# Performance work log

Hardware: AMD Instinct MI355X
Metric: run time of the kernel (lower is better)

The kernel has to match this reference:

```python
import jax, jax.numpy as jnp
import numpy as np

B, NPG, H, HEADS, L, E, IN_DIM, FREQ = 4, 256, 128, 4, 6, 65536, 5, 256
N = B * NPG
C = H // HEADS  # per-head channels = 32


def _w(key, shape, fan_in):
    return jax.random.normal(key, shape, jnp.float32) * (fan_in ** -0.5)


def _ln(x):  # LayerNorm, elementwise_affine=False, eps=1e-5
    mu = jnp.mean(x, axis=-1, keepdims=True)
    var = jnp.mean((x - mu) ** 2, axis=-1, keepdims=True)
    return (x - mu) / jnp.sqrt(var + 1e-5)


def setup_inputs() -> dict:
    key = jax.random.key(0)
    ks = jax.random.split(key, 40)
    x = jax.random.normal(ks[0], (N, IN_DIM), jnp.float32)
    # edges constrained within each graph
    kg = jnp.repeat(jnp.arange(B), E // B)
    src = jax.random.randint(ks[1], (E,), 0, NPG) + kg * NPG
    dst = jax.random.randint(ks[2], (E,), 0, NPG) + kg * NPG
    edge_index = jnp.stack([src, dst]).astype(jnp.int32)
    batch = jnp.repeat(jnp.arange(B), NPG).astype(jnp.int32)
    time_matrix = jax.random.normal(ks[3], (N, N), jnp.float32)
    p = {}
    p['Wn'] = _w(ks[4], (IN_DIM, H), IN_DIM); p['bn'] = jnp.zeros((H,), jnp.float32)
    p['Wee'] = _w(ks[5], (1, 1), 1); p['bee'] = jnp.zeros((1,), jnp.float32)
    p['Wt1'] = _w(ks[6], (FREQ, H), FREQ); p['bt1'] = jnp.zeros((H,), jnp.float32)
    p['Wt2'] = _w(ks[7], (H, H), H); p['bt2'] = jnp.zeros((H,), jnp.float32)
    p['Wa'] = _w(ks[8], (L, H, 4 * H), H); p['ba'] = jnp.zeros((L, 4 * H), jnp.float32)
    p['Wq'] = _w(ks[9], (L, H, H), H); p['bq'] = jnp.zeros((L, H), jnp.float32)
    p['Wk'] = _w(ks[10], (L, H, H), H); p['bk'] = jnp.zeros((L, H), jnp.float32)
    p['Wv'] = _w(ks[11], (L, H, H), H); p['bv'] = jnp.zeros((L, H), jnp.float32)
    p['We'] = _w(ks[12], (L, 1, H), 1)  # lin_edge, bias=False in PyG
    p['Wskip'] = _w(ks[13], (L, H, H), H); p['bskip'] = jnp.zeros((L, H), jnp.float32)
    p['Wf1'] = _w(ks[14], (L, H, 2 * H), H); p['bf1'] = jnp.zeros((L, 2 * H), jnp.float32)
    p['Wf2'] = _w(ks[15], (L, 2 * H, H), 2 * H); p['bf2'] = jnp.zeros((L, H), jnp.float32)
    p['Wb'] = _w(ks[16], (H, H, H), H); p['bb'] = jnp.zeros((H,), jnp.float32)
    p['Wm1'] = _w(ks[17], (H, H), H); p['bm1'] = jnp.zeros((H,), jnp.float32)
    p['Wm2'] = _w(ks[18], (H, 4), H); p['bm2'] = jnp.zeros((4,), jnp.float32)
    return {'x': x, 'edge_index': edge_index, 'batch': batch, 't': 50,
            'time_matrix': time_matrix, **p}


def reference(x, edge_index, batch, t, time_matrix,
              Wn, bn, Wee, bee, Wt1, bt1, Wt2, bt2,
              Wa, ba, Wq, bq, Wk, bk, Wv, bv, We, Wskip, bskip,
              Wf1, bf1, Wf2, bf2, Wb, bb, Wm1, bm1, Wm2, bm2):
    h = x @ Wn + bn  # [N,H]
    # sinusoidal timestep embedding (dim=FREQ)
    half = FREQ // 2
    freqs = jnp.exp(-jnp.log(jnp.float32(10000.0)) * jnp.arange(half, dtype=jnp.float32) / half)
    targs = jnp.float32(t) * freqs
    emb = jnp.concatenate([jnp.cos(targs), jnp.sin(targs)])[None, :]  # [1,FREQ]
    t_emb = jax.nn.silu(emb @ Wt1 + bt1) @ Wt2 + bt2  # [1,H]
    t_mod = jax.nn.silu(t_emb)

    src, dst = edge_index[0], edge_index[1]
    edge_attr = time_matrix[src, dst][:, None] @ Wee + bee  # [E,1]

    inv_sqrt_c = jnp.float32(1.0 / np.sqrt(C))
    for l in range(L):
        ss = t_mod @ Wa[l] + ba[l]  # [1,4H]
        sh_msa, sc_msa, sh_mlp, sc_mlp = jnp.split(ss, 4, axis=1)
        hn = _ln(h) * (1 + sc_msa) + sh_msa
        # TransformerConv: gather per-edge Q/K/V, softmax over incoming edges of dst
        q = (hn @ Wq[l] + bq[l]).reshape(N, HEADS, C)
        k = (hn @ Wk[l] + bk[l]).reshape(N, HEADS, C)
        v = (hn @ Wv[l] + bv[l]).reshape(N, HEADS, C)
        e = (edge_attr @ We[l]).reshape(E, HEADS, C)
        kj = k[src] + e
        alpha = jnp.sum(q[dst] * kj, axis=-1) * inv_sqrt_c  # [E,HEADS]
        m = jax.ops.segment_max(alpha, dst, num_segments=N)
        a = jnp.exp(alpha - m[dst])
        s = jax.ops.segment_sum(a, dst, num_segments=N)
        a = a / (s[dst] + 1e-16)
        msg = (v[src] + e) * a[..., None]  # [E,HEADS,C]
        attn_out = jax.ops.segment_sum(msg, dst, num_segments=N).reshape(N, H)
        attn_out = attn_out + hn @ Wskip[l] + bskip[l]  # root/skip connection
        h = h + attn_out
        hn = _ln(h) * (1 + sc_mlp) + sh_mlp
        h = h + (jax.nn.gelu(hn @ Wf1[l] + bf1[l], approximate=False) @ Wf2[l] + bf2[l])

    # to_dense_batch: all graphs have NPG nodes -> reshape, full mask
    hd = h.reshape(B, NPG, H)
    # nn.Bilinear: pair[b,i,j,o] = h[b,i] @ Wb[o] @ h[b,j] + bb[o]
    tmp = jnp.einsum('bik,okl->biol', hd, Wb)  # [B,n,H,H]
    pair = jnp.einsum('biol,bjl->bijo', tmp, hd) + bb  # [B,n,n,H]
    logits = jax.nn.silu(pair @ Wm1 + bm1) @ Wm2 + bm2  # [B,n,n,4]
    return logits
```

## Files before the change

kernel.cpp:

```cpp
#include <hip/hip_runtime.h>
#include <math.h>

#define N_NODES 1024
#define HDIM 128
#define EDGES 65536
#define LAYERS 6

typedef __attribute__((ext_vector_type(8))) short bf16x8;
typedef __attribute__((ext_vector_type(4))) float f32x4;

#define OFF_H     0
#define OFF_Q     131072
#define OFF_K     262144
#define OFF_V     393216
#define OFF_SKP   524288
#define OFF_G     655360
#define OFF_SS    917504
#define OFF_EA    920576
#define OFF_CVEC  986112
#define OFF_INT   986240
#define OFF_M     1054912
#define OFF_U     3152064
#define OFF_MT    11540672
#define OFF_HB    12589248
#define OFF_TMOD  12654784
#define OFF_WB    12654912

__device__ __forceinline__ float silu_f(float x) { return x / (1.f + expf(-x)); }
__device__ __forceinline__ float frcp(float x) { return __builtin_amdgcn_rcpf(x); }

__device__ __forceinline__ unsigned short f2bf(float f) {
    unsigned int u = __float_as_uint(f);
    u += 0x7FFFu + ((u >> 16) & 1u);
    return (unsigned short)(u >> 16);
}

__global__ __launch_bounds__(1024) void k_tmod(const void* tptr,
    const float* __restrict__ Wt1, const float* __restrict__ bt1,
    const float* __restrict__ Wt2, const float* __restrict__ bt2,
    const float* __restrict__ bb, const float* __restrict__ Wm1, const float* __restrict__ bm1,
    float* __restrict__ tmod_g, float* __restrict__ cvec)
{
    __shared__ float emb_s[256];
    __shared__ float part[8][128];
    __shared__ float tmp1_s[128];
    int tid = threadIdx.x;
    int iv = *(const int*)tptr;
    float fv = __int_as_float(iv);
    float tval = (iv > -1000000 && iv < 1000000) ? (float)iv : fv;
    if (tid < 256) {
        int fi = tid & 127;
        float fr = expf(-logf(10000.f) * (float)fi / 128.f);
        float ta = tval * fr;
        emb_s[tid] = (tid < 128) ? cosf(ta) : sinf(ta);
    }
    __syncthreads();
    {
        int col = tid & 127, sl = tid >> 7;
        float p = 0.f;
#pragma unroll 8
        for (int i = sl * 32; i < sl * 32 + 32; i++) p += emb_s[i] * Wt1[i * 128 + col];
        part[sl][col] = p;
    }
    __syncthreads();
    if (tid < 128) {
        float a = bt1[tid];
#pragma unroll
        for (int s = 0; s < 8; s++) a += part[s][tid];
        tmp1_s[tid] = silu_f(a);
    }
    __syncthreads();
    {
        int col = tid & 127, sl = tid >> 7;
        float p = 0.f;
#pragma unroll 8
        for (int i = sl * 16; i < sl * 16 + 16; i++) p += tmp1_s[i] * Wt2[i * 128 + col];
        part[sl][col] = p;
    }
    __syncthreads();
    if (tid < 128) {
        float a = bt2[tid];
#pragma unroll
        for (int s = 0; s < 8; s++) a += part[s][tid];
        tmod_g[tid] = silu_f(a);
    }
    __syncthreads();
    {
        int col = tid & 127, sl = tid >> 7;
        float p = 0.f;
#pragma unroll 8
        for (int i = sl * 16; i < sl * 16 + 16; i++) p += bb[i] * Wm1[i * 128 + col];
        part[sl][col] = p;
    }
    __syncthreads();
    if (tid < 128) {
        float a = bm1[tid];
#pragma unroll
        for (int s = 0; s < 8; s++) a += part[s][tid];
        cvec[tid] = a;
    }
}

__global__ __launch_bounds__(256) void k_ss(const float* __restrict__ tmod_g,
    const float* __restrict__ Wa, const float* __restrict__ ba, float* __restrict__ ss_all)
{
    __shared__ float tm_s[128];
    int tid = threadIdx.x;
    if (tid < 128) tm_s[tid] = tmod_g[tid];
    __syncthreads();
    int idx = blockIdx.x * 256 + tid;
    int l = idx >> 9, j = idx & 511;
    float a = ba[l * 512 + j];
    const float* w = Wa + l * 65536 + j;
#pragma unroll 4
    for (int k = 0; k < 128; k++) a += tm_s[k] * w[k * 512];
    ss_all[idx] = a;
}

__global__ __launch_bounds__(256) void k_wtrans(
    const float* __restrict__ Wq, const float* __restrict__ Wk,
    const float* __restrict__ Wv, const float* __restrict__ Wsk,
    const float* __restrict__ Wf1, const float* __restrict__ Wf2,
    short* __restrict__ WT)
{
    __shared__ __align__(16) short T[64][80];
    int t = blockIdx.x;
    int tid = threadIdx.x;
    const float* src; short* dst; int K, N, kt, nt;
    if (t < 96) {
        int mat = t >> 2, sub = t & 3;
        int l = mat >> 2, m = mat & 3;
        src = (m == 0 ? Wq : m == 1 ? Wk : m == 2 ? Wv : Wsk) + l * 16384;
        dst = WT + (size_t)mat * 16384;
        K = 128; N = 128; kt = sub >> 1; nt = sub & 1;
    } else if (t < 144) {
        int i = t - 96; int l = i >> 3, sub = i & 7;
        src = Wf1 + l * 32768;
        dst = WT + 24 * 16384 + (size_t)l * 32768;
        K = 128; N = 256; kt = sub & 1; nt = sub >> 1;
    } else {
        int i = t - 144; int l = i >> 3, sub = i & 7;
        src = Wf2 + l * 32768;
        dst = WT + 24 * 16384 + 6 * 32768 + (size_t)l * 32768;
        K = 256; N = 128; kt = sub >> 1; nt = sub & 1;
    }
    int k0 = kt * 64, n0 = nt * 64;
    for (int p = 0; p < 16; p++) {
        int idx = p * 256 + tid;
        int kk = idx >> 6, nn = idx & 63;
        T[nn][kk] = (short)f2bf(src[(k0 + kk) * N + n0 + nn]);
    }
    __syncthreads();
    for (int p = 0; p < 2; p++) {
        int idx = p * 256 + tid;
        int nn = idx >> 3, sq = idx & 7;
        *(int4*)&dst[(size_t)(n0 + nn) * K + k0 + sq * 8] = *(const int4*)&T[nn][sq * 8];
    }
}

__global__ __launch_bounds__(256) void k_input(const float* __restrict__ x,
    const float* __restrict__ Wn, const float* __restrict__ bn, float* __restrict__ h)
{
    int idx = blockIdx.x * 256 + threadIdx.x;
    int i = idx >> 7, j = idx & 127;
    float acc = bn[j];
#pragma unroll
    for (int kk = 0; kk < 5; kk++) acc += x[i * 5 + kk] * Wn[kk * 128 + j];
    h[idx] = acc;
}

__global__ __launch_bounds__(256) void k_edge_count(const int* __restrict__ ei,
    const float* __restrict__ tm, const float* __restrict__ Wee, const float* __restrict__ bee,
    float* __restrict__ ea, int* __restrict__ deg)
{
    int e = blockIdx.x * 256 + threadIdx.x;
    int s = ei[e], d = ei[EDGES + e];
    ea[e] = tm[s * N_NODES + d] * Wee[0] + bee[0];
    atomicAdd(&deg[d], 1);
}

__global__ __launch_bounds__(1024) void k_scan(const int* __restrict__ deg, int* __restrict__ rowptr)
{
    __shared__ int tmp[1024];
    int tid = threadIdx.x;
    tmp[tid] = deg[tid];
    __syncthreads();
    for (int off = 1; off < 1024; off <<= 1) {
        int vv = (tid >= off) ? tmp[tid - off] : 0;
        __syncthreads();
        tmp[tid] += vv;
        __syncthreads();
    }
    rowptr[tid + 1] = tmp[tid];
    if (tid == 0) rowptr[0] = 0;
}

__global__ __launch_bounds__(256) void k_scatter(const int* __restrict__ ei,
    const int* __restrict__ rowptr, int* __restrict__ cursor, int* __restrict__ eorder)
{
    int e = blockIdx.x * 256 + threadIdx.x;
    int d = ei[EDGES + e];
    int pos = atomicAdd(&cursor[d], 1);
    eorder[rowptr[d] + pos] = e;
}

__global__ __launch_bounds__(128) void k_sort2(const int* __restrict__ rowptr,
    int* __restrict__ eorder, const int* __restrict__ ei, const float* __restrict__ ea,
    int* __restrict__ src_csr, float* __restrict__ ea_csr)
{
    __shared__ int key[256];
    int node = blockIdx.x;
    int tid = threadIdx.x;
    int beg = rowptr[node], end = rowptr[node + 1];
    int n = end - beg;
    if (n <= 256) {
        for (int i = tid; i < 256; i += 128) key[i] = (i < n) ? eorder[beg + i] : 0x7FFFFFFF;
        __syncthreads();
        for (int k = 2; k <= 256; k <<= 1) {
            for (int j = k >> 1; j > 0; j >>= 1) {
                int i = ((tid / j) * 2 * j) + (tid % j);
                int l = i + j;
                bool up = ((i & k) == 0);
                int a = key[i], b = key[l];
                if ((a > b) == up) { key[i] = b; key[l] = a; }
                __syncthreads();
            }
        }
        for (int i = tid; i < n; i += 128) {
            int e = key[i];
            src_csr[beg + i] = ei[e];
            ea_csr[beg + i] = ea[e];
        }
    } else {
        if (tid == 0) {
            for (int i = beg + 1; i < end; ++i) {
                int kk = eorder[i];
                int j = i - 1;
                while (j >= beg && eorder[j] > kk) { eorder[j + 1] = eorder[j]; --j; }
                eorder[j + 1] = kk;
            }
        }
        __syncthreads();
        for (int i = tid; i < n; i += 128) {
            int e = eorder[beg + i];
            src_csr[beg + i] = ei[e];
            ea_csr[beg + i] = ea[e];
        }
    }
}

__global__ __launch_bounds__(256) void k_qkvs(const float* __restrict__ h,
    const float* __restrict__ ss, const short* __restrict__ WT, int layer,
    const float* __restrict__ bq, const float* __restrict__ bk,
    const float* __restrict__ bv, const float* __restrict__ bsk,
    float* __restrict__ q, float* __restrict__ k, float* __restrict__ v, float* __restrict__ skp)
{
    __shared__ __align__(16) short As[32][136];
    __shared__ float shs[128], scs[128];
    int tid = threadIdx.x;
    int r0 = blockIdx.x * 32;
    int mat = blockIdx.y;
    if (tid < 128) { shs[tid] = ss[tid]; scs[tid] = ss[128 + tid]; }
    __syncthreads();
    {
        int row = tid >> 3, o = tid & 7;
        const float* hr = h + (size_t)(r0 + row) * 128 + o * 16;
        float s = 0.f, s2 = 0.f;
#pragma unroll
        for (int j = 0; j < 4; j++) {
            float4 vv = *(const float4*)&hr[j * 4];
            s += vv.x + vv.y + vv.z + vv.w;
            s2 += vv.x * vv.x + vv.y * vv.y + vv.z * vv.z + vv.w * vv.w;
        }
        s += __shfl_xor(s, 1, 64); s2 += __shfl_xor(s2, 1, 64);
        s += __shfl_xor(s, 2, 64); s2 += __shfl_xor(s2, 2, 64);
        s += __shfl_xor(s, 4, 64); s2 += __shfl_xor(s2, 4, 64);
        float mu = s * (1.f / 128.f);
        float var = s2 * (1.f / 128.f) - mu * mu;
        float rs = rsqrtf(var + 1e-5f);
#pragma unroll
        for (int j = 0; j < 4; j++) {
            float4 vv = *(const float4*)&hr[j * 4];
            int cb = o * 16 + j * 4;
            short4 o4;
            o4.x = (short)f2bf((vv.x - mu) * rs * (1.f + scs[cb])     + shs[cb]);
            o4.y = (short)f2bf((vv.y - mu) * rs * (1.f + scs[cb + 1]) + shs[cb + 1]);
            o4.z = (short)f2bf((vv.z - mu) * rs * (1.f + scs[cb + 2]) + shs[cb + 2]);
            o4.w = (short)f2bf((vv.w - mu) * rs * (1.f + scs[cb + 3]) + shs[cb + 3]);
            *(short4*)&As[row][cb] = o4;
        }
    }
    __syncthreads();
    int w = tid >> 6, lane = tid & 63, c = lane & 15, g = lane >> 4;
    const short* Wm = WT + (size_t)(layer * 4 + mat) * 16384;
    f32x4 acc[2][2] = {};
#pragma unroll
    for (int kq = 0; kq < 4; kq++) {
        int ko = kq * 32 + g * 8;
        bf16x8 a0 = *(const bf16x8*)&As[c][ko];
        bf16x8 a1 = *(const bf16x8*)&As[16 + c][ko];
#pragma unroll
        for (int nt = 0; nt < 2; nt++) {
            bf16x8 bfr = *(const bf16x8*)&Wm[(size_t)(w * 32 + nt * 16 + c) * 128 + ko];
            acc[0][nt] = __builtin_amdgcn_mfma_f32_16x16x32_bf16(a0, bfr, acc[0][nt], 0, 0, 0);
            acc[1][nt] = __builtin_amdgcn_mfma_f32_16x16x32_bf16(a1, bfr, acc[1][nt], 0, 0, 0);
        }
    }
    const float* bias; float* out;
    switch (mat) {
        case 0:  bias = bq;  out = q;   break;
        case 1:  bias = bk;  out = k;   break;
        case 2:  bias = bv;  out = v;   break;
        default: bias = bsk; out = skp; break;
    }
#pragma unroll
    for (int it = 0; it < 2; it++)
#pragma unroll
        for (int nt = 0; nt < 2; nt++) {
            int n = w * 32 + nt * 16 + c;
            float bv2 = bias[n];
#pragma unroll
            for (int r = 0; r < 4; r++) {
                int i = r0 + it * 16 + g * 4 + r;
                out[(size_t)i * 128 + n] = acc[it][nt][r] + bv2;
            }
        }
}

__global__ __launch_bounds__(256) void k_ffn(float* __restrict__ h,
    const short* __restrict__ WT, int layer,
    const float* __restrict__ bf1, const float* __restrict__ bf2,
    const float* __restrict__ ss2, short* __restrict__ hb, int last)
{
    __shared__ __align__(16) short As[16][136];
    __shared__ __align__(16) short Gs[16][264];
    __shared__ float shs[128], scs[128];
    int tid = threadIdx.x;
    int r0 = blockIdx.x * 16;
    if (tid < 128) { shs[tid] = ss2[tid]; scs[tid] = ss2[128 + tid]; }
    __syncthreads();
    {
        int row = tid >> 4, o = tid & 15;
        const float* hr = h + (size_t)(r0 + row) * 128 + o * 8;
        float s = 0.f, s2 = 0.f;
#pragma unroll
        for (int j = 0; j < 2; j++) {
            float4 vv = *(const float4*)&hr[j * 4];
            s += vv.x + vv.y + vv.z + vv.w;
            s2 += vv.x * vv.x + vv.y * vv.y + vv.z * vv.z + vv.w * vv.w;
        }
        s += __shfl_xor(s, 1, 64); s2 += __shfl_xor(s2, 1, 64);
        s += __shfl_xor(s, 2, 64); s2 += __shfl_xor(s2, 2, 64);
        s += __shfl_xor(s, 4, 64); s2 += __shfl_xor(s2, 4, 64);
        s += __shfl_xor(s, 8, 64); s2 += __shfl_xor(s2, 8, 64);
        float mu = s * (1.f / 128.f);
        float var = s2 * (1.f / 128.f) - mu * mu;
        float rs = rsqrtf(var + 1e-5f);
#pragma unroll
        for (int j = 0; j < 2; j++) {
            float4 vv = *(const float4*)&hr[j * 4];
            int cb = o * 8 + j * 4;
            short4 o4;
            o4.x = (short)f2bf((vv.x - mu) * rs * (1.f + scs[cb])     + shs[cb]);
            o4.y = (short)f2bf((vv.y - mu) * rs * (1.f + scs[cb + 1]) + shs[cb + 1]);
            o4.z = (short)f2bf((vv.z - mu) * rs * (1.f + scs[cb + 2]) + shs[cb + 2]);
            o4.w = (short)f2bf((vv.w - mu) * rs * (1.f + scs[cb + 3]) + shs[cb + 3]);
            *(short4*)&As[row][cb] = o4;
        }
    }
    __syncthreads();
    int w = tid >> 6, lane = tid & 63, c = lane & 15, g = lane >> 4;
    const short* W1 = WT + 24 * 16384 + (size_t)layer * 32768;
    const short* W2 = WT + 24 * 16384 + 6 * 32768 + (size_t)layer * 32768;
    {
        f32x4 acc[4] = {};
#pragma unroll
        for (int kq = 0; kq < 4; kq++) {
            int ko = kq * 32 + g * 8;
            bf16x8 a0 = *(const bf16x8*)&As[c][ko];
#pragma unroll
            for (int nt = 0; nt < 4; nt++) {
                bf16x8 bfr = *(const bf16x8*)&W1[(size_t)(w * 64 + nt * 16 + c) * 128 + ko];
                acc[nt] = __builtin_amdgcn_mfma_f32_16x16x32_bf16(a0, bfr, acc[nt], 0, 0, 0);
            }
        }
#pragma unroll
        for (int nt = 0; nt < 4; nt++) {
            int n = w * 64 + nt * 16 + c;
            float bv = bf1[n];
#pragma unroll
            for (int r = 0; r < 4; r++) {
                float y = acc[nt][r] + bv;
                float gl = 0.5f * y * (1.f + erff(y * 0.70710678118654752f));
                Gs[g * 4 + r][n] = (short)f2bf(gl);
            }
        }
    }
    __syncthreads();
    {
        f32x4 acc2[2] = {};
#pragma unroll
        for (int kq = 0; kq < 8; kq++) {
            int ko = kq * 32 + g * 8;
            bf16x8 a0 = *(const bf16x8*)&Gs[c][ko];
#pragma unroll
            for (int nt2 = 0; nt2 < 2; nt2++) {
                bf16x8 bfr = *(const bf16x8*)&W2[(size_t)(w * 32 + nt2 * 16 + c) * 256 + ko];
                acc2[nt2] = __builtin_amdgcn_mfma_f32_16x16x32_bf16(a0, bfr, acc2[nt2], 0, 0, 0);
            }
        }
#pragma unroll
        for (int nt2 = 0; nt2 < 2; nt2++) {
            int n = w * 32 + nt2 * 16 + c;
            float bv = bf2[n];
#pragma unroll
            for (int r = 0; r < 4; r++) {
                int i = r0 + g * 4 + r;
                float nv = h[(size_t)i * 128 + n] + acc2[nt2][r] + bv;
                h[(size_t)i * 128 + n] = nv;
                if (last) hb[(size_t)i * 128 + n] = (short)f2bf(nv);
            }
        }
    }
}

__global__ __launch_bounds__(256) void k_attn(const float* __restrict__ q,
    const float* __restrict__ k, const float* __restrict__ v,
    const float* __restrict__ skp, float* __restrict__ h,
    const int* __restrict__ src_csr, const float* __restrict__ ea_csr,
    const float* __restrict__ We_l, const int* __restrict__ rowptr)
{
    __shared__ float ms[2][64], ssb[2][64], a0s[2][64], a1s[2][64];
    int tid = threadIdx.x;
    int wid = tid >> 6;
    int lane = tid & 63;
    int nslot = wid >> 1;
    int half = wid & 1;
    int node = blockIdx.x * 2 + nslot;
    int c0 = lane * 2;
    float2 q2 = *(const float2*)&q[node * 128 + c0];
    float we0 = We_l[c0], we1 = We_l[c0 + 1];
    int beg = rowptr[node], end = rowptr[node + 1];
    int n = end - beg;
    int mid = beg + ((n + 1) >> 1);
    int tb = half ? mid : beg;
    int te = half ? end : mid;
    float m = -INFINITY, s = 0.f, a0 = 0.f, a1 = 0.f;
    const float isc = 0.17677669529663687f;

    int t = tb;
    for (; t + 3 < te; t += 4) {
        int sn0 = src_csr[t],     sn1 = src_csr[t + 1];
        int sn2 = src_csr[t + 2], sn3 = src_csr[t + 3];
        float e0 = ea_csr[t],     e1 = ea_csr[t + 1];
        float e2 = ea_csr[t + 2], e3 = ea_csr[t + 3];
        float2 k0 = *(const float2*)&k[sn0 * 128 + c0];
        float2 k1 = *(const float2*)&k[sn1 * 128 + c0];
        float2 k2 = *(const float2*)&k[sn2 * 128 + c0];
        float2 k3 = *(const float2*)&k[sn3 * 128 + c0];
        float2 v0 = *(const float2*)&v[sn0 * 128 + c0];
        float2 v1 = *(const float2*)&v[sn1 * 128 + c0];
        float2 v2 = *(const float2*)&v[sn2 * 128 + c0];
        float2 v3 = *(const float2*)&v[sn3 * 128 + c0];
        float p0 = q2.x * (k0.x + e0 * we0) + q2.y * (k0.y + e0 * we1);
        float p1 = q2.x * (k1.x + e1 * we0) + q2.y * (k1.y + e1 * we1);
        float p2 = q2.x * (k2.x + e2 * we0) + q2.y * (k2.y + e2 * we1);
        float p3 = q2.x * (k3.x + e3 * we0) + q2.y * (k3.y + e3 * we1);
        p0 += __shfl_xor(p0, 1, 16); p1 += __shfl_xor(p1, 1, 16);
        p2 += __shfl_xor(p2, 1, 16); p3 += __shfl_xor(p3, 1, 16);
        p0 += __shfl_xor(p0, 2, 16); p1 += __shfl_xor(p1, 2, 16);
        p2 += __shfl_xor(p2, 2, 16); p3 += __shfl_xor(p3, 2, 16);
        p0 += __shfl_xor(p0, 4, 16); p1 += __shfl_xor(p1, 4, 16);
        p2 += __shfl_xor(p2, 4, 16); p3 += __shfl_xor(p3, 4, 16);
        p0 += __shfl_xor(p0, 8, 16); p1 += __shfl_xor(p1, 8, 16);
        p2 += __shfl_xor(p2, 8, 16); p3 += __shfl_xor(p3, 8, 16);
        {
            float al = p0 * isc;
            float mn = fmaxf(m, al);
            float scale = __expf(m - mn), wq = __expf(al - mn);
            s = s * scale + wq;
            a0 = a0 * scale + wq * (v0.x + e0 * we0);
            a1 = a1 * scale + wq * (v0.y + e0 * we1);
            m = mn;
        }
        {
            float al = p1 * isc;
            float mn = fmaxf(m, al);
            float scale = __expf(m - mn), wq = __expf(al - mn);
            s = s * scale + wq;
            a0 = a0 * scale + wq * (v1.x + e1 * we0);
            a1 = a1 * scale + wq * (v1.y + e1 * we1);
            m = mn;
        }
        {
            float al = p2 * isc;
            float mn = fmaxf(m, al);
            float scale = __expf(m - mn), wq = __expf(al - mn);
            s = s * scale + wq;
            a0 = a0 * scale + wq * (v2.x + e2 * we0);
            a1 = a1 * scale + wq * (v2.y + e2 * we1);
            m = mn;
        }
        {
            float al = p3 * isc;
            float mn = fmaxf(m, al);
            float scale = __expf(m - mn), wq = __expf(al - mn);
            s = s * scale + wq;
            a0 = a0 * scale + wq * (v3.x + e3 * we0);
            a1 = a1 * scale + wq * (v3.y + e3 * we1);
            m = mn;
        }
    }
    for (; t < te; ++t) {
        int sn = src_csr[t];
        float eav = ea_csr[t];
        float2 kv = *(const float2*)&k[sn * 128 + c0];
        float2 vv = *(const float2*)&v[sn * 128 + c0];
        float part = q2.x * (kv.x + eav * we0) + q2.y * (kv.y + eav * we1);
        part += __shfl_xor(part, 1, 16);
        part += __shfl_xor(part, 2, 16);
        part += __shfl_xor(part, 4, 16);
        part += __shfl_xor(part, 8, 16);
        float alpha = part * isc;
        float mn = fmaxf(m, alpha);
        float scale = __expf(m - mn), wq = __expf(alpha - mn);
        s = s * scale + wq;
        a0 = a0 * scale + wq * (vv.x + eav * we0);
        a1 = a1 * scale + wq * (vv.y + eav * we1);
        m = mn;
    }
    if (half == 1) {
        ms[nslot][lane] = m; ssb[nslot][lane] = s;
        a0s[nslot][lane] = a0; a1s[nslot][lane] = a1;
    }
    __syncthreads();
    if (half == 0) {
        float mB = ms[nslot][lane], sB = ssb[nslot][lane];
        float b0 = a0s[nslot][lane], b1 = a1s[nslot][lane];
        float mm = fmaxf(m, mB);
        float eA = (m  > -1e30f) ? __expf(m  - mm) : 0.f;
        float eB = (mB > -1e30f) ? __expf(mB - mm) : 0.f;
        float sT = s * eA + sB * eB;
        float o0 = a0 * eA + b0 * eB;
        float o1 = a1 * eA + b1 * eB;
        float inv = (sT > 0.f) ? 1.f / (sT + 1e-16f) : 0.f;
        int o = node * 128 + c0;
        h[o]     += skp[o]     + o0 * inv;
        h[o + 1] += skp[o + 1] + o1 * inv;
    }
}

__global__ __launch_bounds__(256) void k_mprep(const float* __restrict__ Wb,
    const float* __restrict__ Wm1, float* __restrict__ M)
{
    __shared__ float wb_s[64][128];
    __shared__ float wm_s[64][128];
    int tid = threadIdx.x;
    int k = blockIdx.x;
    int mg = tid & 15, lg = tid >> 4;
    int m0 = mg * 8, l0 = lg * 8;
    float acc[8][8] = {};
    for (int oh = 0; oh < 2; ++oh) {
        __syncthreads();
        for (int idx = tid; idx < 8192; idx += 256) {
            int o = idx >> 7, c = idx & 127;
            wb_s[o][c] = Wb[(size_t)(oh * 64 + o) * 16384 + k * 128 + c];
            wm_s[o][c] = Wm1[(oh * 64 + o) * 128 + c];
        }
        __syncthreads();
        for (int o = 0; o < 64; o++) {
            float lv[8], mv[8];
#pragma unroll
            for (int i = 0; i < 8; i++) { lv[i] = wb_s[o][l0 + i]; mv[i] = wm_s[o][m0 + i]; }
#pragma unroll
            for (int li = 0; li < 8; li++)
#pragma unroll
                for (int mi = 0; mi < 8; mi++) acc[li][mi] += lv[li] * mv[mi];
        }
    }
    for (int mi = 0; mi < 8; mi++)
        for (int li = 0; li < 8; li++)
            M[(size_t)k * 16384 + (m0 + mi) * 128 + (l0 + li)] = acc[li][mi];
}

__global__ __launch_bounds__(256) void k_mtrans(const float* __restrict__ M,
                                                short* __restrict__ Mt)
{
    __shared__ __align__(16) short Ts[64][136];
    int tid = threadIdx.x;
    int n0 = blockIdx.x * 64;
    for (int p = 0; p < 32; p++) {
        int idx = p * 256 + tid;
        int k = idx >> 6, nn = idx & 63;
        Ts[nn][k] = (short)f2bf(M[(size_t)k * 16384 + n0 + nn]);
    }
    __syncthreads();
    for (int p = 0; p < 4; p++) {
        int idx = p * 256 + tid;
        int nn = idx >> 4, s = idx & 15;
        *(int4*)&Mt[(size_t)(n0 + nn) * 128 + s * 8] = *(const int4*)&Ts[nn][s * 8];
    }
}

__global__ __launch_bounds__(256) void k_p1(const short* __restrict__ hb,
    const short* __restrict__ Mt, short* __restrict__ U)
{
    __shared__ __align__(16) short As[128][72];
    __shared__ __align__(16) short Bs[128][72];
    int tid = threadIdx.x;
    int n0 = blockIdx.x * 128;
    int i0 = blockIdx.y * 128;
    int w = tid >> 6, lane = tid & 63, c = lane & 15, g = lane >> 4;
    f32x4 acc[2][8] = {};
    for (int kh = 0; kh < 2; kh++) {
        __syncthreads();
        for (int idx = tid; idx < 1024; idx += 256) {
            int r = idx >> 3, s = idx & 7;
            *(int4*)&As[r][s * 8] = *(const int4*)&hb[(i0 + r) * 128 + kh * 64 + s * 8];
            *(int4*)&Bs[r][s * 8] = *(const int4*)&Mt[(size_t)(n0 + r) * 128 + kh * 64 + s * 8];
        }
        __syncthreads();
#pragma unroll
        for (int kk = 0; kk < 2; kk++) {
            int ko = kk * 32 + g * 8;
            bf16x8 a0 = *(const bf16x8*)&As[w * 32 + c][ko];
            bf16x8 a1 = *(const bf16x8*)&As[w * 32 + 16 + c][ko];
#pragma unroll
            for (int nt = 0; nt < 8; nt++) {
                bf16x8 b = *(const bf16x8*)&Bs[nt * 16 + c][ko];
                acc[0][nt] = __builtin_amdgcn_mfma_f32_16x16x32_bf16(a0, b, acc[0][nt], 0, 0, 0);
                acc[1][nt] = __builtin_amdgcn_mfma_f32_16x16x32_bf16(a1, b, acc[1][nt], 0, 0, 0);
            }
        }
    }
#pragma unroll
    for (int it = 0; it < 2; it++)
#pragma unroll
        for (int nt = 0; nt < 8; nt++)
#pragma unroll
            for (int r = 0; r < 4; r++) {
                int i = i0 + w * 32 + it * 16 + g * 4 + r;
                int n = n0 + nt * 16 + c;
                U[(size_t)i * 16384 + n] = (short)f2bf(acc[it][nt][r]);
            }
}

__global__ __launch_bounds__(256) void k_p2(const short* __restrict__ hb,
    const short* __restrict__ U, const float* __restrict__ cvec,
    const float* __restrict__ Wm2, const float* __restrict__ bm2,
    float* __restrict__ out)
{
    __shared__ __align__(16) short Us[128][136];
    __shared__ float cvs[128];
    __shared__ float w2s[128][4];
    int tid = threadIdx.x;
    int i = blockIdx.x;
    int jb = blockIdx.y;
    int b = i >> 8;
    int w = tid >> 6, lane = tid & 63, c = lane & 15, g = lane >> 4;
    if (tid < 128) {
        cvs[tid] = cvec[tid];
        *(float4*)&w2s[tid][0] = *(const float4*)&Wm2[tid * 4];
    }
    bf16x8 hf[2][4];
    {
        const short* hrow = hb + (size_t)(b * 256 + jb * 128 + w * 32 + c) * 128;
#pragma unroll
        for (int jt = 0; jt < 2; jt++)
#pragma unroll
            for (int kq = 0; kq < 4; kq++)
                hf[jt][kq] = *(const bf16x8*)(hrow + jt * 16 * 128 + kq * 32 + g * 8);
    }
    for (int idx = tid; idx < 2048; idx += 256) {
        int r = idx >> 4, s = idx & 15;
        *(int4*)&Us[r][s * 8] = *(const int4*)&U[(size_t)i * 16384 + r * 128 + s * 8];
    }
    __syncthreads();
    f32x4 acc[2][8] = {};
#pragma unroll
    for (int kq = 0; kq < 4; kq++) {
        int ko = kq * 32 + g * 8;
#pragma unroll
        for (int mt = 0; mt < 8; mt++) {
            bf16x8 uv = *(const bf16x8*)&Us[mt * 16 + c][ko];
            acc[0][mt] = __builtin_amdgcn_mfma_f32_16x16x32_bf16(uv, hf[0][kq], acc[0][mt], 0, 0, 0);
            acc[1][mt] = __builtin_amdgcn_mfma_f32_16x16x32_bf16(uv, hf[1][kq], acc[1][mt], 0, 0, 0);
        }
    }
    float4 bmv = *(const float4*)&bm2[0];
#pragma unroll
    for (int jt = 0; jt < 2; jt++) {
        float p0 = 0.f, p1 = 0.f, p2 = 0.f, p3 = 0.f;
#pragma unroll
        for (int mt = 0; mt < 8; mt++) {
#pragma unroll
            for (int r = 0; r < 4; r++) {
                int m = mt * 16 + g * 4 + r;
                float y = acc[jt][mt][r] + cvs[m];
                float sv = y * frcp(1.f + __expf(-y));
                p0 += sv * w2s[m][0]; p1 += sv * w2s[m][1];
                p2 += sv * w2s[m][2]; p3 += sv * w2s[m][3];
            }
        }
        p0 += __shfl_xor(p0, 16, 64); p1 += __shfl_xor(p1, 16, 64);
        p2 += __shfl_xor(p2, 16, 64); p3 += __shfl_xor(p3, 16, 64);
        p0 += __shfl_xor(p0, 32, 64); p1 += __shfl_xor(p1, 32, 64);
        p2 += __shfl_xor(p2, 32, 64); p3 += __shfl_xor(p3, 32, 64);
        if (g == 0) {
            int j = jb * 128 + w * 32 + jt * 16 + c;
            float4 o4 = { p0 + bmv.x, p1 + bmv.y, p2 + bmv.z, p3 + bmv.w };
            *(float4*)&out[((size_t)i * 256 + j) * 4] = o4;
        }
    }
}

extern "C" void kernel_launch(void* const* d_in, const int* in_sizes, int n_in,
                              void* d_out, int out_size, void* d_ws, size_t ws_size,
                              hipStream_t stream)
{
    const float* x   = (const float*)d_in[0];
    const int*   ei  = (const int*)d_in[1];
    const void*  tptr= d_in[3];
    const float* tm  = (const float*)d_in[4];
    const float* Wn  = (const float*)d_in[5];
    const float* bn  = (const float*)d_in[6];
    const float* Wee = (const float*)d_in[7];
    const float* bee = (const float*)d_in[8];
    const float* Wt1 = (const float*)d_in[9];
    const float* bt1 = (const float*)d_in[10];
    const float* Wt2 = (const float*)d_in[11];
    const float* bt2 = (const float*)d_in[12];
    const float* Wa  = (const float*)d_in[13];
    const float* ba  = (const float*)d_in[14];
    const float* Wq  = (const float*)d_in[15];
    const float* bq  = (const float*)d_in[16];
    const float* Wk  = (const float*)d_in[17];
    const float* bk  = (const float*)d_in[18];
    const float* Wv  = (const float*)d_in[19];
    const float* bv  = (const float*)d_in[20];
    const float* We  = (const float*)d_in[21];
    const float* Wsk = (const float*)d_in[22];
    const float* bsk = (const float*)d_in[23];
    const float* Wf1 = (const float*)d_in[24];
    const float* bf1 = (const float*)d_in[25];
    const float* Wf2 = (const float*)d_in[26];
    const float* bf2 = (const float*)d_in[27];
    const float* Wb  = (const float*)d_in[28];
    const float* bb  = (const float*)d_in[29];
    const float* Wm1 = (const float*)d_in[30];
    const float* bm1 = (const float*)d_in[31];
    const float* Wm2 = (const float*)d_in[32];
    const float* bm2 = (const float*)d_in[33];
    float* out = (float*)d_out;
    float* ws = (float*)d_ws;

    float* h    = ws + OFF_H;
    float* qb   = ws + OFF_Q;
    float* kb   = ws + OFF_K;
    float* vb   = ws + OFF_V;
    float* skp  = ws + OFF_SKP;
    float* ss   = ws + OFF_SS;
    float* ea   = ws + OFF_EA;
    float* cvec = ws + OFF_CVEC;
    int* iws    = (int*)(ws + OFF_INT);
    int* deg    = iws;
    int* cursor = iws + 1024;
    int* rowptr = iws + 2048;
    int* eorder = iws + 3073;
    int* src_csr   = (int*)(ws + OFF_G);
    float* ea_csr  = ws + OFF_G + 65536;
    float* Mst  = ws + OFF_M;
    short* Ub   = (short*)(ws + OFF_U);
    short* Mtb  = (short*)(ws + OFF_MT);
    short* hbb  = (short*)(ws + OFF_HB);
    float* tmod = ws + OFF_TMOD;
    short* WT   = (short*)(ws + OFF_WB);

    hipMemsetAsync(deg, 0, 2048 * sizeof(int), stream);
    k_tmod<<<1, 1024, 0, stream>>>(tptr, Wt1, bt1, Wt2, bt2, bb, Wm1, bm1, tmod, cvec);
    k_ss<<<12, 256, 0, stream>>>(tmod, Wa, ba, ss);
    k_wtrans<<<192, 256, 0, stream>>>(Wq, Wk, Wv, Wsk, Wf1, Wf2, WT);
    k_input<<<512, 256, 0, stream>>>(x, Wn, bn, h);
    k_edge_count<<<256, 256, 0, stream>>>(ei, tm, Wee, bee, ea, deg);
    k_scan<<<1, 1024, 0, stream>>>(deg, rowptr);
    k_scatter<<<256, 256, 0, stream>>>(ei, rowptr, cursor, eorder);
    k_sort2<<<1024, 128, 0, stream>>>(rowptr, eorder, ei, ea, src_csr, ea_csr);

    for (int l = 0; l < LAYERS; l++) {
        const float* ssl = ss + l * 512;
        k_qkvs<<<dim3(32, 4), 256, 0, stream>>>(h, ssl, WT, l,
            bq + l * 128, bk + l * 128, bv + l * 128, bsk + l * 128,
            qb, kb, vb, skp);
        k_attn<<<512, 256, 0, stream>>>(qb, kb, vb, skp, h, src_csr, ea_csr,
                                        We + l * 128, rowptr);
        k_ffn<<<64, 256, 0, stream>>>(h, WT, l, bf1 + l * 256, bf2 + l * 128,
                                      ssl + 256, hbb, l == LAYERS - 1);
    }

    k_mprep<<<128, 256, 0, stream>>>(Wb, Wm1, Mst);
    k_mtrans<<<256, 256, 0, stream>>>(Mst, Mtb);
    k_p1<<<dim3(128, 8), 256, 0, stream>>>(hbb, Mtb, Ub);
    k_p2<<<dim3(1024, 2), 256, 0, stream>>>(hbb, Ub, cvec, Wm2, bm2, out);
}
```

Measured before the change: 286.8 us.

## Fuse setup kernels, split attention per node over four waves, use MFMA for bilinear prep

Merges the time-embedding and scale/shift kernels into one 12-block launch, and the input projection and edge-count kernels into one launch, to cut launch overhead. Each node's attention now gets a whole block, with its edges split across four waves and merged by online softmax. The bilinear weight precompute becomes a bf16 MFMA GEMM that reads a transposed bf16 Wm1 written by the weight-transpose kernel. Each fused setup block recomputes the time MLP redundantly, and bf16 lowers the precision of the bilinear weights.

```diff
diff --git a/kernel.cpp b/kernel.cpp
--- a/kernel.cpp
+++ b/kernel.cpp
@@ -26,6 +26,8 @@
 #define OFF_TMOD  12654784
 #define OFF_WB    12654912
 
+#define WM1T_OFF  786432
+
 __device__ __forceinline__ float silu_f(float x) { return x / (1.f + expf(-x)); }
 __device__ __forceinline__ float frcp(float x) { return __builtin_amdgcn_rcpf(x); }
 
@@ -35,20 +37,22 @@
     return (unsigned short)(u >> 16);
 }
 
-__global__ __launch_bounds__(1024) void k_tmod(const void* tptr,
+__global__ __launch_bounds__(256) void k_ssf(const void* tptr,
     const float* __restrict__ Wt1, const float* __restrict__ bt1,
     const float* __restrict__ Wt2, const float* __restrict__ bt2,
     const float* __restrict__ bb, const float* __restrict__ Wm1, const float* __restrict__ bm1,
-    float* __restrict__ tmod_g, float* __restrict__ cvec)
+    const float* __restrict__ Wa, const float* __restrict__ ba,
+    float* __restrict__ ss_all, float* __restrict__ cvec)
 {
     __shared__ float emb_s[256];
-    __shared__ float part[8][128];
+    __shared__ float part[2][128];
     __shared__ float tmp1_s[128];
+    __shared__ float tmod_s[128];
     int tid = threadIdx.x;
     int iv = *(const int*)tptr;
     float fv = __int_as_float(iv);
     float tval = (iv > -1000000 && iv < 1000000) ? (float)iv : fv;
-    if (tid < 256) {
+    {
         int fi = tid & 127;
         float fr = expf(-logf(10000.f) * (float)fi / 128.f);
         float ta = tval * fr;
@@ -59,69 +63,49 @@
         int col = tid & 127, sl = tid >> 7;
         float p = 0.f;
 #pragma unroll 8
-        for (int i = sl * 32; i < sl * 32 + 32; i++) p += emb_s[i] * Wt1[i * 128 + col];
+        for (int i = sl * 128; i < sl * 128 + 128; i++) p += emb_s[i] * Wt1[i * 128 + col];
         part[sl][col] = p;
     }
     __syncthreads();
-    if (tid < 128) {
-        float a = bt1[tid];
-#pragma unroll
-        for (int s = 0; s < 8; s++) a += part[s][tid];
-        tmp1_s[tid] = silu_f(a);
-    }
+    if (tid < 128) tmp1_s[tid] = silu_f(bt1[tid] + part[0][tid] + part[1][tid]);
     __syncthreads();
     {
         int col = tid & 127, sl = tid >> 7;
         float p = 0.f;
 #pragma unroll 8
-        for (int i = sl * 16; i < sl * 16 + 16; i++) p += tmp1_s[i] * Wt2[i * 128 + col];
+        for (int i = sl * 64; i < sl * 64 + 64; i++) p += tmp1_s[i] * Wt2[i * 128 + col];
         part[sl][col] = p;
     }
     __syncthreads();
-    if (tid < 128) {
-        float a = bt2[tid];
-#pragma unroll
-        for (int s = 0; s < 8; s++) a += part[s][tid];
-        tmod_g[tid] = silu_f(a);
-    }
-    __syncthreads();
-    {
-        int col = tid & 127, sl = tid >> 7;
-        float p = 0.f;
+    if (tid < 128) tmod_s[tid] = silu_f(bt2[tid] + part[0][tid] + part[1][tid]);
+    __syncthreads();
+    {
+        int idx = blockIdx.x * 256 + tid;
+        int l = idx >> 9, j = idx & 511;
+        float a = ba[l * 512 + j];
+        const float* w = Wa + l * 65536 + j;
+#pragma unroll 4
+        for (int k = 0; k < 128; k++) a += tmod_s[k] * w[k * 512];
+        ss_all[idx] = a;
+    }
+    if (blockIdx.x == 0) {
+        {
+            int col = tid & 127, sl = tid >> 7;
+            float p = 0.f;
 #pragma unroll 8
-        for (int i = sl * 16; i < sl * 16 + 16; i++) p += bb[i] * Wm1[i * 128 + col];
-        part[sl][col] = p;
-    }
-    __syncthreads();
-    if (tid < 128) {
-        float a = bm1[tid];
-#pragma unroll
-        for (int s = 0; s < 8; s++) a += part[s][tid];
-        cvec[tid] = a;
-    }
-}
-
-__global__ __launch_bounds__(256) void k_ss(const float* __restrict__ tmod_g,
-    const float* __restrict__ Wa, const float* __restrict__ ba, float* __restrict__ ss_all)
-{
-    __shared__ float tm_s[128];
-    int tid = threadIdx.x;
-    if (tid < 128) tm_s[tid] = tmod_g[tid];
-    __syncthreads();
-    int idx = blockIdx.x * 256 + tid;
-    int l = idx >> 9, j = idx & 511;
-    float a = ba[l * 512 + j];
-    const float* w = Wa + l * 65536 + j;
-#pragma unroll 4
-    for (int k = 0; k < 128; k++) a += tm_s[k] * w[k * 512];
-    ss_all[idx] = a;
+            for (int i = sl * 64; i < sl * 64 + 64; i++) p += bb[i] * Wm1[i * 128 + col];
+            part[sl][col] = p;
+        }
+        __syncthreads();
+        if (tid < 128) cvec[tid] = bm1[tid] + part[0][tid] + part[1][tid];
+    }
 }
 
 __global__ __launch_bounds__(256) void k_wtrans(
     const float* __restrict__ Wq, const float* __restrict__ Wk,
     const float* __restrict__ Wv, const float* __restrict__ Wsk,
     const float* __restrict__ Wf1, const float* __restrict__ Wf2,
-    short* __restrict__ WT)
+    const float* __restrict__ Wm1, short* __restrict__ WT)
 {
     __shared__ __align__(16) short T[64][80];
     int t = blockIdx.x;
@@ -138,11 +122,16 @@
         src = Wf1 + l * 32768;
         dst = WT + 24 * 16384 + (size_t)l * 32768;
         K = 128; N = 256; kt = sub & 1; nt = sub >> 1;
-    } else {
+    } else if (t < 192) {
         int i = t - 144; int l = i >> 3, sub = i & 7;
         src = Wf2 + l * 32768;
         dst = WT + 24 * 16384 + 6 * 32768 + (size_t)l * 32768;
         K = 256; N = 128; kt = sub >> 1; nt = sub & 1;
+    } else {
+        int sub = t - 192;
+        src = Wm1;
+        dst = WT + WM1T_OFF;
+        K = 128; N = 128; kt = sub >> 1; nt = sub & 1;
     }
     int k0 = kt * 64, n0 = nt * 64;
     for (int p = 0; p < 16; p++) {
@@ -158,25 +147,27 @@
     }
 }
 
-__global__ __launch_bounds__(256) void k_input(const float* __restrict__ x,
-    const float* __restrict__ Wn, const float* __restrict__ bn, float* __restrict__ h)
-{
-    int idx = blockIdx.x * 256 + threadIdx.x;
-    int i = idx >> 7, j = idx & 127;
-    float acc = bn[j];
-#pragma unroll
-    for (int kk = 0; kk < 5; kk++) acc += x[i * 5 + kk] * Wn[kk * 128 + j];
-    h[idx] = acc;
-}
-
-__global__ __launch_bounds__(256) void k_edge_count(const int* __restrict__ ei,
-    const float* __restrict__ tm, const float* __restrict__ Wee, const float* __restrict__ bee,
+__global__ __launch_bounds__(256) void k_inpedge(const float* __restrict__ x,
+    const float* __restrict__ Wn, const float* __restrict__ bn, float* __restrict__ h,
+    const int* __restrict__ ei, const float* __restrict__ tm,
+    const float* __restrict__ Wee, const float* __restrict__ bee,
     float* __restrict__ ea, int* __restrict__ deg)
 {
-    int e = blockIdx.x * 256 + threadIdx.x;
-    int s = ei[e], d = ei[EDGES + e];
-    ea[e] = tm[s * N_NODES + d] * Wee[0] + bee[0];
-    atomicAdd(&deg[d], 1);
+    int bid = blockIdx.x;
+    int tid = threadIdx.x;
+    if (bid < 512) {
+        int idx = bid * 256 + tid;
+        int i = idx >> 7, j = idx & 127;
+        float acc = bn[j];
+#pragma unroll
+        for (int kk = 0; kk < 5; kk++) acc += x[i * 5 + kk] * Wn[kk * 128 + j];
+        h[idx] = acc;
+    } else {
+        int e = (bid - 512) * 256 + tid;
+        int s = ei[e], d = ei[EDGES + e];
+        ea[e] = tm[s * N_NODES + d] * Wee[0] + bee[0];
+        atomicAdd(&deg[d], 1);
+    }
 }
 
 __global__ __launch_bounds__(1024) void k_scan(const int* __restrict__ deg, int* __restrict__ rowptr)
@@ -430,21 +421,18 @@
     const int* __restrict__ src_csr, const float* __restrict__ ea_csr,
     const float* __restrict__ We_l, const int* __restrict__ rowptr)
 {
-    __shared__ float ms[2][64], ssb[2][64], a0s[2][64], a1s[2][64];
+    __shared__ float ms[3][64], ssb[3][64], a0s[3][64], a1s[3][64];
     int tid = threadIdx.x;
     int wid = tid >> 6;
     int lane = tid & 63;
-    int nslot = wid >> 1;
-    int half = wid & 1;
-    int node = blockIdx.x * 2 + nslot;
+    int node = blockIdx.x;
     int c0 = lane * 2;
     float2 q2 = *(const float2*)&q[node * 128 + c0];
     float we0 = We_l[c0], we1 = We_l[c0 + 1];
     int beg = rowptr[node], end = rowptr[node + 1];
     int n = end - beg;
-    int mid = beg + ((n + 1) >> 1);
-    int tb = half ? mid : beg;
-    int te = half ? end : mid;
+    int tb = beg + (n * wid) / 4;
+    int te = beg + (n * (wid + 1)) / 4;
     float m = -INFINITY, s = 0.f, a0 = 0.f, a1 = 0.f;
     const float isc = 0.17677669529663687f;
 
@@ -529,58 +517,76 @@
         a1 = a1 * scale + wq * (vv.y + eav * we1);
         m = mn;
     }
-    if (half == 1) {
-        ms[nslot][lane] = m; ssb[nslot][lane] = s;
-        a0s[nslot][lane] = a0; a1s[nslot][lane] = a1;
-    }
-    __syncthreads();
-    if (half == 0) {
-        float mB = ms[nslot][lane], sB = ssb[nslot][lane];
-        float b0 = a0s[nslot][lane], b1 = a1s[nslot][lane];
-        float mm = fmaxf(m, mB);
-        float eA = (m  > -1e30f) ? __expf(m  - mm) : 0.f;
-        float eB = (mB > -1e30f) ? __expf(mB - mm) : 0.f;
-        float sT = s * eA + sB * eB;
-        float o0 = a0 * eA + b0 * eB;
-        float o1 = a1 * eA + b1 * eB;
-        float inv = (sT > 0.f) ? 1.f / (sT + 1e-16f) : 0.f;
+    if (wid > 0) {
+        ms[wid - 1][lane] = m; ssb[wid - 1][lane] = s;
+        a0s[wid - 1][lane] = a0; a1s[wid - 1][lane] = a1;
+    }
+    __syncthreads();
+    if (wid == 0) {
+#pragma unroll
+        for (int p = 0; p < 3; p++) {
+            float mB = ms[p][lane], sB = ssb[p][lane];
+            float b0 = a0s[p][lane], b1 = a1s[p][lane];
+            float mm = fmaxf(m, mB);
+            float eA = (m  > -1e30f) ? __expf(m  - mm) : 0.f;
+            float eB = (mB > -1e30f) ? __expf(mB - mm) : 0.f;
+            s = s * eA + sB * eB;
+            a0 = a0 * eA + b0 * eB;
+            a1 = a1 * eA + b1 * eB;
+            m = mm;
+        }
+        float inv = (s > 0.f) ? 1.f / (s + 1e-16f) : 0.f;
         int o = node * 128 + c0;
-        h[o]     += skp[o]     + o0 * inv;
-        h[o + 1] += skp[o + 1] + o1 * inv;
+        h[o]     += skp[o]     + a0 * inv;
+        h[o + 1] += skp[o + 1] + a1 * inv;
     }
 }
 
 __global__ __launch_bounds__(256) void k_mprep(const float* __restrict__ Wb,
-    const float* __restrict__ Wm1, float* __restrict__ M)
-{
-    __shared__ float wb_s[64][128];
-    __shared__ float wm_s[64][128];
+    const short* __restrict__ WT, float* __restrict__ M)
+{
+    __shared__ __align__(16) short Bls[128][136];
     int tid = threadIdx.x;
     int k = blockIdx.x;
-    int mg = tid & 15, lg = tid >> 4;
-    int m0 = mg * 8, l0 = lg * 8;
-    float acc[8][8] = {};
-    for (int oh = 0; oh < 2; ++oh) {
-        __syncthreads();
-        for (int idx = tid; idx < 8192; idx += 256) {
-            int o = idx >> 7, c = idx & 127;
-            wb_s[o][c] = Wb[(size_t)(oh * 64 + o) * 16384 + k * 128 + c];
-            wm_s[o][c] = Wm1[(oh * 64 + o) * 128 + c];
-        }
-        __syncthreads();
-        for (int o = 0; o < 64; o++) {
-            float lv[8], mv[8];
-#pragma unroll
-            for (int i = 0; i < 8; i++) { lv[i] = wb_s[o][l0 + i]; mv[i] = wm_s[o][m0 + i]; }
-#pragma unroll
-            for (int li = 0; li < 8; li++)
-#pragma unroll
-                for (int mi = 0; mi < 8; mi++) acc[li][mi] += lv[li] * mv[mi];
-        }
-    }
-    for (int mi = 0; mi < 8; mi++)
-        for (int li = 0; li < 8; li++)
-            M[(size_t)k * 16384 + (m0 + mi) * 128 + (l0 + li)] = acc[li][mi];
+    const short* Wm1T = WT + WM1T_OFF;
+    {
+        int lq = (tid & 31) * 4;
+        int ob = tid >> 5;
+        for (int it = 0; it < 16; it++) {
+            int o = it * 8 + ob;
+            float4 vv = *(const float4*)&Wb[(size_t)o * 16384 + k * 128 + lq];
+            Bls[lq][o]     = (short)f2bf(vv.x);
+            Bls[lq + 1][o] = (short)f2bf(vv.y);
+            Bls[lq + 2][o] = (short)f2bf(vv.z);
+            Bls[lq + 3][o] = (short)f2bf(vv.w);
+        }
+    }
+    __syncthreads();
+    int w = tid >> 6, lane = tid & 63, c = lane & 15, g = lane >> 4;
+    f32x4 acc[2][8] = {};
+#pragma unroll
+    for (int kq = 0; kq < 4; kq++) {
+        int ko = kq * 32 + g * 8;
+        bf16x8 a0 = *(const bf16x8*)&Wm1T[(size_t)(w * 32 + c) * 128 + ko];
+        bf16x8 a1 = *(const bf16x8*)&Wm1T[(size_t)(w * 32 + 16 + c) * 128 + ko];
+#pragma unroll
+        for (int nt = 0; nt < 8; nt++) {
+            bf16x8 b = *(const bf16x8*)&Bls[nt * 16 + c][ko];
+            acc[0][nt] = __builtin_amdgcn_mfma_f32_16x16x32_bf16(a0, b, acc[0][nt], 0, 0, 0);
+            acc[1][nt] = __builtin_amdgcn_mfma_f32_16x16x32_bf16(a1, b, acc[1][nt], 0, 0, 0);
+        }
+    }
+    float* Mk = M + (size_t)k * 16384;
+#pragma unroll
+    for (int it = 0; it < 2; it++)
+#pragma unroll
+        for (int nt = 0; nt < 8; nt++)
+#pragma unroll
+            for (int r = 0; r < 4; r++) {
+                int m = w * 32 + it * 16 + g * 4 + r;
+                int l = nt * 16 + c;
+                Mk[m * 128 + l] = acc[it][nt][r];
+            }
 }
 
 __global__ __launch_bounds__(256) void k_mtrans(const float* __restrict__ M,
@@ -773,15 +779,12 @@
     short* Ub   = (short*)(ws + OFF_U);
     short* Mtb  = (short*)(ws + OFF_MT);
     short* hbb  = (short*)(ws + OFF_HB);
-    float* tmod = ws + OFF_TMOD;
     short* WT   = (short*)(ws + OFF_WB);
 
     hipMemsetAsync(deg, 0, 2048 * sizeof(int), stream);
-    k_tmod<<<1, 1024, 0, stream>>>(tptr, Wt1, bt1, Wt2, bt2, bb, Wm1, bm1, tmod, cvec);
-    k_ss<<<12, 256, 0, stream>>>(tmod, Wa, ba, ss);
-    k_wtrans<<<192, 256, 0, stream>>>(Wq, Wk, Wv, Wsk, Wf1, Wf2, WT);
-    k_input<<<512, 256, 0, stream>>>(x, Wn, bn, h);
-    k_edge_count<<<256, 256, 0, stream>>>(ei, tm, Wee, bee, ea, deg);
+    k_ssf<<<12, 256, 0, stream>>>(tptr, Wt1, bt1, Wt2, bt2, bb, Wm1, bm1, Wa, ba, ss, cvec);
+    k_wtrans<<<196, 256, 0, stream>>>(Wq, Wk, Wv, Wsk, Wf1, Wf2, Wm1, WT);
+    k_inpedge<<<768, 256, 0, stream>>>(x, Wn, bn, h, ei, tm, Wee, bee, ea, deg);
     k_scan<<<1, 1024, 0, stream>>>(deg, rowptr);
     k_scatter<<<256, 256, 0, stream>>>(ei, rowptr, cursor, eorder);
     k_sort2<<<1024, 128, 0, stream>>>(rowptr, eorder, ei, ea, src_csr, ea_csr);
@@ -791,13 +794,13 @@
         k_qkvs<<<dim3(32, 4), 256, 0, stream>>>(h, ssl, WT, l,
             bq + l * 128, bk + l * 128, bv + l * 128, bsk + l * 128,
             qb, kb, vb, skp);
-        k_attn<<<512, 256, 0, stream>>>(qb, kb, vb, skp, h, src_csr, ea_csr,
-                                        We + l * 128, rowptr);
+        k_attn<<<1024, 256, 0, stream>>>(qb, kb, vb, skp, h, src_csr, ea_csr,
+                                         We + l * 128, rowptr);
         k_ffn<<<64, 256, 0, stream>>>(h, WT, l, bf1 + l * 256, bf2 + l * 128,
                                       ssl + 256, hbb, l == LAYERS - 1);
     }
 
-    k_mprep<<<128, 256, 0, stream>>>(Wb, Wm1, Mst);
+    k_mprep<<<128, 256, 0, stream>>>(Wb, WT, Mst);
     k_mtrans<<<256, 256, 0, stream>>>(Mst, Mtb);
     k_p1<<<dim3(128, 8), 256, 0, stream>>>(hbb, Mtb, Ub);
     k_p2<<<dim3(1024, 2), 256, 0, stream>>>(hbb, Ub, cvec, Wm2, bm2, out);
```

Measured after the change: 266.3 us. 1.08x faster.
